# Performance work log

Hardware: AMD Instinct MI355X
Metric: run time of the kernel (lower is better)

Reference implementation:

```python
import jax, jax.numpy as jnp
import numpy as np

SEQ, B, D_IN, D_H = 512, 64, 512, 512


def setup_inputs() -> dict:
    key = jax.random.key(0)
    ks = jax.random.split(key, 5)
    s = 1.0 / np.sqrt(D_IN + D_H)
    inp = {
        "inputs": jax.random.normal(ks[0], (SEQ, B, D_IN), dtype=jnp.float32),
        "W_f": jax.random.normal(ks[1], (D_H, D_IN + D_H), dtype=jnp.float32) * s,
        "b_f": jnp.zeros((D_H,), jnp.float32),
        "W_i": jax.random.normal(ks[2], (D_H, D_IN + D_H), dtype=jnp.float32) * s,
        "b_i": jnp.zeros((D_H,), jnp.float32),
        "W_g": jax.random.normal(ks[3], (D_H, D_IN + D_H), dtype=jnp.float32) * s,
        "b_g": jnp.zeros((D_H,), jnp.float32),
        "W_o": jax.random.normal(ks[4], (D_H, D_IN + D_H), dtype=jnp.float32) * s,
        "b_o": jnp.zeros((D_H,), jnp.float32),
    }
    return inp


def reference(inputs, W_f, b_f, W_i, b_i, W_g, b_g, W_o, b_o):
    # inputs: [seq, batch, d_in]; states start at zeros (module default)
    B_ = inputs.shape[1]
    h0 = jnp.zeros((B_, D_H), inputs.dtype)
    c0 = jnp.zeros((B_, D_H), inputs.dtype)

    def step(carry, x_t):
        hx, cx = carry
        combined = jnp.concatenate([x_t, hx], axis=1)  # [B, d_in+d_h]
        f = jax.nn.sigmoid(combined @ W_f.T + b_f)
        i = jax.nn.sigmoid(combined @ W_i.T + b_i)
        g = jnp.tanh(combined @ W_g.T + b_g)
        o = jax.nn.sigmoid(combined @ W_o.T + b_o)
        cx = f * cx + i * g
        hx = o * jnp.tanh(cx)
        return (hx, cx), hx

    (hx, cx), stacked = jax.lax.scan(step, (h0, c0), inputs)
    return stacked, hx, cx
```

## Files before the change

### kernel.cpp

```cpp
#include <hip/hip_runtime.h>

#define SEQ   512
#define BATCH 64
#define DIN   512
#define DH    512
#define KTOT  1024
#define NWG   128
#define NTH   256
#define HBUF_BYTES 65536

#define FLAGS_BYTES 65536
#define HBASE_OFF   65536
#define XBF_OFF     (HBASE_OFF + 512 * HBUF_BYTES)
#define XBF_BYTES   ((size_t)SEQ * 4 * 16 * 1024)
#define WS_MODE1    ((size_t)HBASE_OFF + 511 * HBUF_BYTES)
#define WS_MODE2    ((size_t)XBF_OFF + XBF_BYTES)
#define FLAG_STRIDE 32

typedef __attribute__((ext_vector_type(8))) short short8;
typedef __attribute__((ext_vector_type(4))) float f32x4;

__device__ __forceinline__ float tanh_fast(float v) {
    const float e = __expf(2.0f * v);
    return 1.0f - 2.0f / (e + 1.0f);
}

__device__ __forceinline__ unsigned int f2bf(float f) {
    unsigned int u = __float_as_uint(f);
    return (u + 0x7fffu + ((u >> 16) & 1u)) >> 16;
}

__device__ __forceinline__ short8 cvt8(float4 lo, float4 hi) {
    short8 r;
    r[0] = (short)f2bf(lo.x); r[1] = (short)f2bf(lo.y);
    r[2] = (short)f2bf(lo.z); r[3] = (short)f2bf(lo.w);
    r[4] = (short)f2bf(hi.x); r[5] = (short)f2bf(hi.y);
    r[6] = (short)f2bf(hi.z); r[7] = (short)f2bf(hi.w);
    return r;
}

__device__ __forceinline__ unsigned int ld_flag(const unsigned int* p) {
    return __hip_atomic_load(p, __ATOMIC_RELAXED, __HIP_MEMORY_SCOPE_AGENT);
}
__device__ __forceinline__ void st_flag(unsigned int* p, unsigned int v) {
    __hip_atomic_store(p, v, __ATOMIC_RELAXED, __HIP_MEMORY_SCOPE_AGENT);
}
__device__ __forceinline__ unsigned long long ld_h_sc1(const unsigned long long* p) {
    return __hip_atomic_load(p, __ATOMIC_RELAXED, __HIP_MEMORY_SCOPE_AGENT);
}
__device__ __forceinline__ void st_h(unsigned long long* p, unsigned long long v) {
    __hip_atomic_store(p, v, __ATOMIC_RELAXED, __HIP_MEMORY_SCOPE_AGENT);
}

__global__ __launch_bounds__(256)
void xconv(const float* __restrict__ x, unsigned short* __restrict__ xbf)
{
    const int gid = blockIdx.x * 256 + threadIdx.x;
    const int l   = gid & 63;
    const int kt  = (gid >> 6) & 15;
    const int mtt = (gid >> 10) & 3;
    const int t   = gid >> 12;
    const float* src = x + ((size_t)t * BATCH + mtt * 16 + (l & 15)) * DIN
                         + kt * 32 + (l >> 4) * 8;
    *(short8*)(xbf + (size_t)gid * 8) =
        cvt8(*(const float4*)src, *(const float4*)(src + 4));
}

template <int MODE>
__global__ __launch_bounds__(NTH, 1)
void lstm_mfma(const float* __restrict__ x,
               const unsigned short* __restrict__ xbf,
               const float* __restrict__ Wf, const float* __restrict__ bfp,
               const float* __restrict__ Wi, const float* __restrict__ bip,
               const float* __restrict__ Wg, const float* __restrict__ bgp,
               const float* __restrict__ Wo, const float* __restrict__ bop,
               float* __restrict__ out,
               unsigned int* __restrict__ ws_u32)
{
    const int tid = threadIdx.x;
    const int l   = tid & 63;
    const int mt  = tid >> 6;
    const int wg  = blockIdx.x;
    const int j0  = wg * 4;

    const int n    = l & 15;
    const int khi  = l >> 4;
    const bool isg = (khi == 2);

    unsigned int* const flags = ws_u32;
    char* const hbase = (char*)ws_u32 + HBASE_OFF;

    const float* Wn = (n < 8) ? ((n < 4) ? Wf : Wi) : ((n < 12) ? Wg : Wo);
    const float* wrow = Wn + (size_t)(j0 + (n & 3)) * KTOT + khi * 8;
    short8 Bfr[32];
    #pragma unroll
    for (int kt = 0; kt < 32; ++kt) {
        Bfr[kt] = cvt8(*(const float4*)(wrow + kt * 32),
                       *(const float4*)(wrow + kt * 32 + 4));
    }
    const float* bptr = (khi == 0) ? bfp : (khi == 1) ? bip : (khi == 2) ? bgp : bop;
    const float4 bias4 = *(const float4*)(bptr + j0);

    float cst0 = 0.f, cst1 = 0.f, cst2 = 0.f, cst3 = 0.f;

    float* const hx_out = out + (size_t)SEQ * BATCH * DH;
    float* const cx_out = hx_out + (size_t)BATCH * DH;

    const int kth         = wg >> 3;
    const int lane_f_base = ((wg & 7) >> 1) << 4;
    const int half8       = (wg & 1) * 8;

    const unsigned int* const f0p = flags + (size_t)l * FLAG_STRIDE;
    const unsigned int* const f1p = f0p + (size_t)64 * FLAG_STRIDE;
    unsigned int* const my_flag = flags + (size_t)wg * FLAG_STRIDE;

    const float*  xrow_base = x + (size_t)(mt * 16 + (l & 15)) * DIN + khi * 8;
    const short8* xbf_base  = (const short8*)xbf + (size_t)mt * 16 * 64 + l;

    for (int t = 0; t < SEQ; ++t) {
        f32x4 acc_a = {0.f, 0.f, 0.f, 0.f};
        f32x4 acc_b = {0.f, 0.f, 0.f, 0.f};

        if (MODE == 2) {
            const short8* xp = xbf_base + (size_t)t * 4096;
            #pragma unroll
            for (int kt = 0; kt < 16; kt += 2) {
                acc_a = __builtin_amdgcn_mfma_f32_16x16x32_bf16(Bfr[kt], xp[kt * 64],
                                                                acc_a, 0, 0, 0);
                acc_b = __builtin_amdgcn_mfma_f32_16x16x32_bf16(Bfr[kt + 1], xp[(kt + 1) * 64],
                                                                acc_b, 0, 0, 0);
            }
        } else {
            const float* xr = xrow_base + (size_t)t * BATCH * DIN;
            #pragma unroll
            for (int kt = 0; kt < 16; kt += 2) {
                const short8 a0 = cvt8(*(const float4*)(xr + kt * 32),
                                       *(const float4*)(xr + kt * 32 + 4));
                const short8 a1 = cvt8(*(const float4*)(xr + (kt + 1) * 32),
                                       *(const float4*)(xr + (kt + 1) * 32 + 4));
                acc_a = __builtin_amdgcn_mfma_f32_16x16x32_bf16(Bfr[kt], a0, acc_a, 0, 0, 0);
                acc_b = __builtin_amdgcn_mfma_f32_16x16x32_bf16(Bfr[kt + 1], a1, acc_b, 0, 0, 0);
            }
        }

        if (t > 0) {
            if (mt == 0) {
                const unsigned int target = (unsigned int)t;
                for (;;) {
                    const unsigned int fa = ld_flag(f0p);
                    const unsigned int fb = ld_flag(f1p);
                    if (__all(fa >= target && fb >= target)) break;
                    __builtin_amdgcn_s_sleep(1);
                }
                asm volatile("" ::: "memory");
            }
            __syncthreads();

            if (MODE == 0) {
                const unsigned long long* hp =
                    (const unsigned long long*)(hbase + ((t & 1) ^ 1) * HBUF_BYTES)
                    + ((size_t)(mt * 16) * 64 + l) * 2;
                #pragma unroll
                for (int kt = 0; kt < 16; kt += 2) {
                    union { unsigned long long u[2]; short8 v; } U0, U1;
                    U0.u[0] = ld_h_sc1(hp + kt * 128);
                    U0.u[1] = ld_h_sc1(hp + kt * 128 + 1);
                    U1.u[0] = ld_h_sc1(hp + (kt + 1) * 128);
                    U1.u[1] = ld_h_sc1(hp + (kt + 1) * 128 + 1);
                    acc_a = __builtin_amdgcn_mfma_f32_16x16x32_bf16(Bfr[16 + kt], U0.v,
                                                                    acc_a, 0, 0, 0);
                    acc_b = __builtin_amdgcn_mfma_f32_16x16x32_bf16(Bfr[17 + kt], U1.v,
                                                                    acc_b, 0, 0, 0);
                }
            } else {
                const uint4* hp = (const uint4*)(hbase + (size_t)(t - 1) * HBUF_BYTES)
                                  + ((size_t)(mt * 16) * 64 + l);
                uint4 hv[16];
                #pragma unroll
                for (int kt = 0; kt < 16; ++kt) hv[kt] = hp[kt * 64];
                #pragma unroll
                for (int kt = 0; kt < 16; kt += 2) {
                    union { uint4 u; short8 v; } U0, U1;
                    U0.u = hv[kt]; U1.u = hv[kt + 1];
                    acc_a = __builtin_amdgcn_mfma_f32_16x16x32_bf16(Bfr[16 + kt], U0.v,
                                                                    acc_a, 0, 0, 0);
                    acc_b = __builtin_amdgcn_mfma_f32_16x16x32_bf16(Bfr[17 + kt], U1.v,
                                                                    acc_b, 0, 0, 0);
                }
            }
        }

        float aq0, aq1, aq2, aq3;
        {
            const float m = isg ? 2.0f : 1.0f;
            const float p0 = acc_a[0] + acc_b[0] + bias4.x;
            const float p1 = acc_a[1] + acc_b[1] + bias4.y;
            const float p2 = acc_a[2] + acc_b[2] + bias4.z;
            const float p3 = acc_a[3] + acc_b[3] + bias4.w;
            const float y0 = 1.0f / (1.0f + __expf(-m * p0));
            const float y1 = 1.0f / (1.0f + __expf(-m * p1));
            const float y2 = 1.0f / (1.0f + __expf(-m * p2));
            const float y3 = 1.0f / (1.0f + __expf(-m * p3));
            aq0 = isg ? 2.0f * y0 - 1.0f : y0;
            aq1 = isg ? 2.0f * y1 - 1.0f : y1;
            aq2 = isg ? 2.0f * y2 - 1.0f : y2;
            aq3 = isg ? 2.0f * y3 - 1.0f : y3;
        }
        const float i0 = __shfl_xor(aq0, 16), g0 = __shfl_xor(aq0, 32), o0 = __shfl_xor(aq0, 48);
        const float i1 = __shfl_xor(aq1, 16), g1 = __shfl_xor(aq1, 32), o1 = __shfl_xor(aq1, 48);
        const float i2 = __shfl_xor(aq2, 16), g2 = __shfl_xor(aq2, 32), o2 = __shfl_xor(aq2, 48);
        const float i3 = __shfl_xor(aq3, 16), g3 = __shfl_xor(aq3, 32), o3 = __shfl_xor(aq3, 48);

        const bool active = (l < 16);
        float hq0 = 0.f, hq1 = 0.f, hq2 = 0.f, hq3 = 0.f;

        if (active) {
            cst0 = fmaf(aq0, cst0, i0 * g0); hq0 = o0 * tanh_fast(cst0);
            cst1 = fmaf(aq1, cst1, i1 * g1); hq1 = o1 * tanh_fast(cst1);
            cst2 = fmaf(aq2, cst2, i2 * g2); hq2 = o2 * tanh_fast(cst2);
            cst3 = fmaf(aq3, cst3, i3 * g3); hq3 = o3 * tanh_fast(cst3);

            if (t < SEQ - 1) {
                const unsigned long long pk =
                    (unsigned long long)(f2bf(hq0) | (f2bf(hq1) << 16))
                    | ((unsigned long long)(f2bf(hq2) | (f2bf(hq3) << 16)) << 32);
                char* const wb = (MODE == 0) ? hbase + (t & 1) * HBUF_BYTES
                                             : hbase + (size_t)t * HBUF_BYTES;
                unsigned long long* hp_w = (unsigned long long*)
                    (wb + (((size_t)(mt * 16 + kth) * 64
                            + (lane_f_base | l)) << 4) + half8);
                st_h(hp_w, pk);
            }
        }

        if (t < SEQ - 1) {
            asm volatile("s_waitcnt vmcnt(0)" ::: "memory");
            __syncthreads();
            if (tid == 0) st_flag(my_flag, (unsigned int)(t + 1));
        }

        if (active) {
            const int b = mt * 16 + l;
            const float4 ov = make_float4(hq0, hq1, hq2, hq3);
            *(float4*)(out + ((size_t)t * BATCH + b) * DH + j0) = ov;
            if (t == SEQ - 1) {
                *(float4*)(hx_out + (size_t)b * DH + j0) = ov;
                *(float4*)(cx_out + (size_t)b * DH + j0) =
                    make_float4(cst0, cst1, cst2, cst3);
            }
        }
    }
}

extern "C" void kernel_launch(void* const* d_in, const int* in_sizes, int n_in,
                              void* d_out, int out_size, void* d_ws, size_t ws_size,
                              hipStream_t stream)
{
    const float* x  = (const float*)d_in[0];
    const float* Wf = (const float*)d_in[1];
    const float* bf = (const float*)d_in[2];
    const float* Wi = (const float*)d_in[3];
    const float* bi = (const float*)d_in[4];
    const float* Wg = (const float*)d_in[5];
    const float* bg = (const float*)d_in[6];
    const float* Wo = (const float*)d_in[7];
    const float* bo = (const float*)d_in[8];
    float* out = (float*)d_out;

    hipMemsetAsync(d_ws, 0, FLAGS_BYTES, stream);

    unsigned int* wsp = (unsigned int*)d_ws;
    if (ws_size >= WS_MODE2) {
        unsigned short* xbf = (unsigned short*)((char*)d_ws + XBF_OFF);
        xconv<<<SEQ * 4 * 16 * 64 / 256, 256, 0, stream>>>(x, xbf);
        lstm_mfma<2><<<NWG, NTH, 0, stream>>>(x, xbf, Wf, bf, Wi, bi,
                                              Wg, bg, Wo, bo, out, wsp);
    } else if (ws_size >= WS_MODE1) {
        lstm_mfma<1><<<NWG, NTH, 0, stream>>>(x, nullptr, Wf, bf, Wi, bi,
                                              Wg, bg, Wo, bo, out, wsp);
    } else {
        lstm_mfma<0><<<NWG, NTH, 0, stream>>>(x, nullptr, Wf, bf, Wi, bi,
                                              Wg, bg, Wo, bo, out, wsp);
    }
}
```

Baseline: 2.286 ms.

## Add dedicated poller wave publishing per-k-tile readiness for incremental h consumption

Adds a fifth wavefront per workgroup that polls the producer flags and publishes a per-k-tile readiness bitmask in shared memory. The four compute waves then consume h tiles and issue their MFMAs as soon as each tile's producers have finished, instead of waiting behind a workgroup barrier for every producer. This is meant to overlap the recurrent matmul with the tail of the cross-workgroup wait. In exchange it adds an extra wave, shared-memory spinning and switch-based dispatch with variable tile order, which may increase register pressure and hurt MFMA scheduling.

```diff
diff --git a/kernel.cpp b/kernel.cpp
--- a/kernel.cpp
+++ b/kernel.cpp
@@ -6,7 +6,7 @@
 #define DH    512
 #define KTOT  1024
 #define NWG   128
-#define NTH   256
+#define NTH   320
 #define HBUF_BYTES 65536
 
 #define FLAGS_BYTES 65536
@@ -77,11 +77,14 @@
                float* __restrict__ out,
                unsigned int* __restrict__ ws_u32)
 {
-    const int tid = threadIdx.x;
-    const int l   = tid & 63;
-    const int mt  = tid >> 6;
-    const int wg  = blockIdx.x;
-    const int j0  = wg * 4;
+    __shared__ unsigned int ready_word;
+
+    const int tid  = threadIdx.x;
+    const int l    = tid & 63;
+    const int mt   = (tid >> 6) & 3;
+    const bool isPoll = (tid >= 256);
+    const int wg   = blockIdx.x;
+    const int j0   = wg * 4;
 
     const int n    = l & 15;
     const int khi  = l >> 4;
@@ -90,16 +93,25 @@
     unsigned int* const flags = ws_u32;
     char* const hbase = (char*)ws_u32 + HBASE_OFF;
 
-    const float* Wn = (n < 8) ? ((n < 4) ? Wf : Wi) : ((n < 12) ? Wg : Wo);
-    const float* wrow = Wn + (size_t)(j0 + (n & 3)) * KTOT + khi * 8;
+    if (tid == 256) {
+        __hip_atomic_store(&ready_word, 0u, __ATOMIC_RELEASE,
+                           __HIP_MEMORY_SCOPE_WORKGROUP);
+    }
+
     short8 Bfr[32];
-    #pragma unroll
-    for (int kt = 0; kt < 32; ++kt) {
-        Bfr[kt] = cvt8(*(const float4*)(wrow + kt * 32),
-                       *(const float4*)(wrow + kt * 32 + 4));
+    float4 bias4 = make_float4(0.f, 0.f, 0.f, 0.f);
+    if (!isPoll) {
+        const float* Wn = (n < 8) ? ((n < 4) ? Wf : Wi) : ((n < 12) ? Wg : Wo);
+        const float* wrow = Wn + (size_t)(j0 + (n & 3)) * KTOT + khi * 8;
+        #pragma unroll
+        for (int kt = 0; kt < 32; ++kt) {
+            Bfr[kt] = cvt8(*(const float4*)(wrow + kt * 32),
+                           *(const float4*)(wrow + kt * 32 + 4));
+        }
+        const float* bptr = (khi == 0) ? bfp : (khi == 1) ? bip
+                          : (khi == 2) ? bgp : bop;
+        bias4 = *(const float4*)(bptr + j0);
     }
-    const float* bptr = (khi == 0) ? bfp : (khi == 1) ? bip : (khi == 2) ? bgp : bop;
-    const float4 bias4 = *(const float4*)(bptr + j0);
 
     float cst0 = 0.f, cst1 = 0.f, cst2 = 0.f, cst3 = 0.f;
 
@@ -120,126 +132,162 @@
     for (int t = 0; t < SEQ; ++t) {
         f32x4 acc_a = {0.f, 0.f, 0.f, 0.f};
         f32x4 acc_b = {0.f, 0.f, 0.f, 0.f};
-
-        if (MODE == 2) {
-            const short8* xp = xbf_base + (size_t)t * 4096;
-            #pragma unroll
-            for (int kt = 0; kt < 16; kt += 2) {
-                acc_a = __builtin_amdgcn_mfma_f32_16x16x32_bf16(Bfr[kt], xp[kt * 64],
-                                                                acc_a, 0, 0, 0);
-                acc_b = __builtin_amdgcn_mfma_f32_16x16x32_bf16(Bfr[kt + 1], xp[(kt + 1) * 64],
-                                                                acc_b, 0, 0, 0);
-            }
-        } else {
-            const float* xr = xrow_base + (size_t)t * BATCH * DIN;
-            #pragma unroll
-            for (int kt = 0; kt < 16; kt += 2) {
-                const short8 a0 = cvt8(*(const float4*)(xr + kt * 32),
-                                       *(const float4*)(xr + kt * 32 + 4));
-                const short8 a1 = cvt8(*(const float4*)(xr + (kt + 1) * 32),
-                                       *(const float4*)(xr + (kt + 1) * 32 + 4));
-                acc_a = __builtin_amdgcn_mfma_f32_16x16x32_bf16(Bfr[kt], a0, acc_a, 0, 0, 0);
-                acc_b = __builtin_amdgcn_mfma_f32_16x16x32_bf16(Bfr[kt + 1], a1, acc_b, 0, 0, 0);
-            }
-        }
-
-        if (t > 0) {
-            if (mt == 0) {
-                const unsigned int target = (unsigned int)t;
-                for (;;) {
-                    const unsigned int fa = ld_flag(f0p);
-                    const unsigned int fb = ld_flag(f1p);
-                    if (__all(fa >= target && fb >= target)) break;
-                    __builtin_amdgcn_s_sleep(1);
-                }
-                asm volatile("" ::: "memory");
-            }
-            __syncthreads();
-
-            if (MODE == 0) {
-                const unsigned long long* hp =
+        float hq0 = 0.f, hq1 = 0.f, hq2 = 0.f, hq3 = 0.f;
+
+        if (!isPoll) {
+            if (MODE == 2) {
+                const short8* xp = xbf_base + (size_t)t * 4096;
+                #pragma unroll
+                for (int kt = 0; kt < 16; kt += 2) {
+                    acc_a = __builtin_amdgcn_mfma_f32_16x16x32_bf16(Bfr[kt], xp[kt * 64],
+                                                                    acc_a, 0, 0, 0);
+                    acc_b = __builtin_amdgcn_mfma_f32_16x16x32_bf16(Bfr[kt + 1], xp[(kt + 1) * 64],
+                                                                    acc_b, 0, 0, 0);
+                }
+            } else {
+                const float* xr = xrow_base + (size_t)t * BATCH * DIN;
+                #pragma unroll
+                for (int kt = 0; kt < 16; kt += 2) {
+                    const short8 a0 = cvt8(*(const float4*)(xr + kt * 32),
+                                           *(const float4*)(xr + kt * 32 + 4));
+                    const short8 a1 = cvt8(*(const float4*)(xr + (kt + 1) * 32),
+                                           *(const float4*)(xr + (kt + 1) * 32 + 4));
+                    acc_a = __builtin_amdgcn_mfma_f32_16x16x32_bf16(Bfr[kt], a0, acc_a, 0, 0, 0);
+                    acc_b = __builtin_amdgcn_mfma_f32_16x16x32_bf16(Bfr[kt + 1], a1, acc_b, 0, 0, 0);
+                }
+            }
+
+            if (t > 0) {
+                const unsigned long long* hp0 =
                     (const unsigned long long*)(hbase + ((t & 1) ^ 1) * HBUF_BYTES)
                     + ((size_t)(mt * 16) * 64 + l) * 2;
+                const uint4* hp1 =
+                    (const uint4*)(hbase + (size_t)(t - 1) * HBUF_BYTES)
+                    + ((size_t)(mt * 16) * 64 + l);
+
+#define CONSUME_KT(KT) {                                                      \
+    union { uint4 u; unsigned long long ul[2]; short8 v; } U;                 \
+    if (MODE == 0) {                                                          \
+        U.ul[0] = ld_h_sc1(hp0 + (KT) * 128);                                 \
+        U.ul[1] = ld_h_sc1(hp0 + (KT) * 128 + 1);                             \
+    } else {                                                                  \
+        U.u = hp1[(KT) * 64];                                                 \
+    }                                                                         \
+    if ((KT) & 1) acc_b = __builtin_amdgcn_mfma_f32_16x16x32_bf16(            \
+                              Bfr[16 + (KT)], U.v, acc_b, 0, 0, 0);           \
+    else          acc_a = __builtin_amdgcn_mfma_f32_16x16x32_bf16(            \
+                              Bfr[16 + (KT)], U.v, acc_a, 0, 0, 0); }
+
+                unsigned int remaining = 0xFFFFu;
+                while (remaining) {
+                    const unsigned int w = __hip_atomic_load(&ready_word,
+                                               __ATOMIC_ACQUIRE,
+                                               __HIP_MEMORY_SCOPE_WORKGROUP);
+                    unsigned int avail = ((w >> 16) == (unsigned int)t)
+                                         ? (w & 0xFFFFu) & remaining : 0u;
+                    if (!avail) { __builtin_amdgcn_s_sleep(1); continue; }
+                    remaining &= ~avail;
+                    do {
+                        const int kt = (int)__builtin_ctz(avail);
+                        avail &= avail - 1;
+                        switch (kt) {
+                            case 0:  CONSUME_KT(0)  break;
+                            case 1:  CONSUME_KT(1)  break;
+                            case 2:  CONSUME_KT(2)  break;
+                            case 3:  CONSUME_KT(3)  break;
+                            case 4:  CONSUME_KT(4)  break;
+                            case 5:  CONSUME_KT(5)  break;
+                            case 6:  CONSUME_KT(6)  break;
+                            case 7:  CONSUME_KT(7)  break;
+                            case 8:  CONSUME_KT(8)  break;
+                            case 9:  CONSUME_KT(9)  break;
+                            case 10: CONSUME_KT(10) break;
+                            case 11: CONSUME_KT(11) break;
+                            case 12: CONSUME_KT(12) break;
+                            case 13: CONSUME_KT(13) break;
+                            case 14: CONSUME_KT(14) break;
+                            default: CONSUME_KT(15) break;
+                        }
+                    } while (avail);
+                }
+#undef CONSUME_KT
+            }
+
+            float aq0, aq1, aq2, aq3;
+            {
+                const float m = isg ? 2.0f : 1.0f;
+                const float p0 = acc_a[0] + acc_b[0] + bias4.x;
+                const float p1 = acc_a[1] + acc_b[1] + bias4.y;
+                const float p2 = acc_a[2] + acc_b[2] + bias4.z;
+                const float p3 = acc_a[3] + acc_b[3] + bias4.w;
+                const float y0 = 1.0f / (1.0f + __expf(-m * p0));
+                const float y1 = 1.0f / (1.0f + __expf(-m * p1));
+                const float y2 = 1.0f / (1.0f + __expf(-m * p2));
+                const float y3 = 1.0f / (1.0f + __expf(-m * p3));
+                aq0 = isg ? 2.0f * y0 - 1.0f : y0;
+                aq1 = isg ? 2.0f * y1 - 1.0f : y1;
+                aq2 = isg ? 2.0f * y2 - 1.0f : y2;
+                aq3 = isg ? 2.0f * y3 - 1.0f : y3;
+            }
+            const float i0 = __shfl_xor(aq0, 16), g0 = __shfl_xor(aq0, 32), o0 = __shfl_xor(aq0, 48);
+            const float i1 = __shfl_xor(aq1, 16), g1 = __shfl_xor(aq1, 32), o1 = __shfl_xor(aq1, 48);
+            const float i2 = __shfl_xor(aq2, 16), g2 = __shfl_xor(aq2, 32), o2 = __shfl_xor(aq2, 48);
+            const float i3 = __shfl_xor(aq3, 16), g3 = __shfl_xor(aq3, 32), o3 = __shfl_xor(aq3, 48);
+
+            if (l < 16) {
+                cst0 = fmaf(aq0, cst0, i0 * g0); hq0 = o0 * tanh_fast(cst0);
+                cst1 = fmaf(aq1, cst1, i1 * g1); hq1 = o1 * tanh_fast(cst1);
+                cst2 = fmaf(aq2, cst2, i2 * g2); hq2 = o2 * tanh_fast(cst2);
+                cst3 = fmaf(aq3, cst3, i3 * g3); hq3 = o3 * tanh_fast(cst3);
+
+                if (t < SEQ - 1) {
+                    const unsigned long long pk =
+                        (unsigned long long)(f2bf(hq0) | (f2bf(hq1) << 16))
+                        | ((unsigned long long)(f2bf(hq2) | (f2bf(hq3) << 16)) << 32);
+                    char* const wb = (MODE == 0) ? hbase + (t & 1) * HBUF_BYTES
+                                                 : hbase + (size_t)t * HBUF_BYTES;
+                    unsigned long long* hp_w = (unsigned long long*)
+                        (wb + (((size_t)(mt * 16 + kth) * 64
+                                + (lane_f_base | l)) << 4) + half8);
+                    st_h(hp_w, pk);
+                }
+            }
+        } else if (t > 0) {
+            const unsigned int target = (unsigned int)t;
+            unsigned int cum = 0;
+            for (;;) {
+                const unsigned int fa = ld_flag(f0p);
+                const unsigned int fb = ld_flag(f1p);
+                const unsigned long long b0 = __ballot(fa >= target);
+                const unsigned long long b1 = __ballot(fb >= target);
+                unsigned int m16 = 0;
                 #pragma unroll
-                for (int kt = 0; kt < 16; kt += 2) {
-                    union { unsigned long long u[2]; short8 v; } U0, U1;
-                    U0.u[0] = ld_h_sc1(hp + kt * 128);
-                    U0.u[1] = ld_h_sc1(hp + kt * 128 + 1);
-                    U1.u[0] = ld_h_sc1(hp + (kt + 1) * 128);
-                    U1.u[1] = ld_h_sc1(hp + (kt + 1) * 128 + 1);
-                    acc_a = __builtin_amdgcn_mfma_f32_16x16x32_bf16(Bfr[16 + kt], U0.v,
-                                                                    acc_a, 0, 0, 0);
-                    acc_b = __builtin_amdgcn_mfma_f32_16x16x32_bf16(Bfr[17 + kt], U1.v,
-                                                                    acc_b, 0, 0, 0);
-                }
-            } else {
-                const uint4* hp = (const uint4*)(hbase + (size_t)(t - 1) * HBUF_BYTES)
-                                  + ((size_t)(mt * 16) * 64 + l);
-                uint4 hv[16];
-                #pragma unroll
-                for (int kt = 0; kt < 16; ++kt) hv[kt] = hp[kt * 64];
-                #pragma unroll
-                for (int kt = 0; kt < 16; kt += 2) {
-                    union { uint4 u; short8 v; } U0, U1;
-                    U0.u = hv[kt]; U1.u = hv[kt + 1];
-                    acc_a = __builtin_amdgcn_mfma_f32_16x16x32_bf16(Bfr[16 + kt], U0.v,
-                                                                    acc_a, 0, 0, 0);
-                    acc_b = __builtin_amdgcn_mfma_f32_16x16x32_bf16(Bfr[17 + kt], U1.v,
-                                                                    acc_b, 0, 0, 0);
-                }
+                for (int g = 0; g < 8; ++g) {
+                    if (((b0 >> (8 * g)) & 0xFFull) == 0xFFull) m16 |= 1u << g;
+                    if (((b1 >> (8 * g)) & 0xFFull) == 0xFFull) m16 |= 1u << (g + 8);
+                }
+                if (m16 != cum) {
+                    cum = m16;
+                    if ((tid & 63) == 0) {
+                        __hip_atomic_store(&ready_word, (target << 16) | cum,
+                                           __ATOMIC_RELEASE,
+                                           __HIP_MEMORY_SCOPE_WORKGROUP);
+                    }
+                }
+                if (cum == 0xFFFFu) break;
+                __builtin_amdgcn_s_sleep(1);
             }
         }
 
-        float aq0, aq1, aq2, aq3;
-        {
-            const float m = isg ? 2.0f : 1.0f;
-            const float p0 = acc_a[0] + acc_b[0] + bias4.x;
-            const float p1 = acc_a[1] + acc_b[1] + bias4.y;
-            const float p2 = acc_a[2] + acc_b[2] + bias4.z;
-            const float p3 = acc_a[3] + acc_b[3] + bias4.w;
-            const float y0 = 1.0f / (1.0f + __expf(-m * p0));
-            const float y1 = 1.0f / (1.0f + __expf(-m * p1));
-            const float y2 = 1.0f / (1.0f + __expf(-m * p2));
-            const float y3 = 1.0f / (1.0f + __expf(-m * p3));
-            aq0 = isg ? 2.0f * y0 - 1.0f : y0;
-            aq1 = isg ? 2.0f * y1 - 1.0f : y1;
-            aq2 = isg ? 2.0f * y2 - 1.0f : y2;
-            aq3 = isg ? 2.0f * y3 - 1.0f : y3;
-        }
-        const float i0 = __shfl_xor(aq0, 16), g0 = __shfl_xor(aq0, 32), o0 = __shfl_xor(aq0, 48);
-        const float i1 = __shfl_xor(aq1, 16), g1 = __shfl_xor(aq1, 32), o1 = __shfl_xor(aq1, 48);
-        const float i2 = __shfl_xor(aq2, 16), g2 = __shfl_xor(aq2, 32), o2 = __shfl_xor(aq2, 48);
-        const float i3 = __shfl_xor(aq3, 16), g3 = __shfl_xor(aq3, 32), o3 = __shfl_xor(aq3, 48);
-
-        const bool active = (l < 16);
-        float hq0 = 0.f, hq1 = 0.f, hq2 = 0.f, hq3 = 0.f;
-
-        if (active) {
-            cst0 = fmaf(aq0, cst0, i0 * g0); hq0 = o0 * tanh_fast(cst0);
-            cst1 = fmaf(aq1, cst1, i1 * g1); hq1 = o1 * tanh_fast(cst1);
-            cst2 = fmaf(aq2, cst2, i2 * g2); hq2 = o2 * tanh_fast(cst2);
-            cst3 = fmaf(aq3, cst3, i3 * g3); hq3 = o3 * tanh_fast(cst3);
-
-            if (t < SEQ - 1) {
-                const unsigned long long pk =
-                    (unsigned long long)(f2bf(hq0) | (f2bf(hq1) << 16))
-                    | ((unsigned long long)(f2bf(hq2) | (f2bf(hq3) << 16)) << 32);
-                char* const wb = (MODE == 0) ? hbase + (t & 1) * HBUF_BYTES
-                                             : hbase + (size_t)t * HBUF_BYTES;
-                unsigned long long* hp_w = (unsigned long long*)
-                    (wb + (((size_t)(mt * 16 + kth) * 64
-                            + (lane_f_base | l)) << 4) + half8);
-                st_h(hp_w, pk);
-            }
-        }
-
         if (t < SEQ - 1) {
-            asm volatile("s_waitcnt vmcnt(0)" ::: "memory");
+            if (!isPoll) {
+                asm volatile("s_waitcnt vmcnt(0)" ::: "memory");
+            }
             __syncthreads();
             if (tid == 0) st_flag(my_flag, (unsigned int)(t + 1));
         }
 
-        if (active) {
+        if (!isPoll && l < 16) {
             const int b = mt * 16 + l;
             const float4 ov = make_float4(hq0, hq1, hq2, hq3);
             *(float4*)(out + ((size_t)t * BATCH + b) * DH + j0) = ov;
```

Measured after the change: 4.295 ms. 1.88x slower.
